# Optimization experiments

Hardware: AMD Instinct MI355X
Metric: run time of the kernel (lower is better)

Reference implementation:

```python
import jax, jax.numpy as jnp
import numpy as np

B, C1, H, W = 8, 256, 192, 192
P = 4              # effective patch size (even, <= H,W)
ROUTE_RATIO = 0.25
MIN_REGIONS = 1
HIDDEN = 128       # max(int(c1*0.5), 16)
ROUTE_HIDDEN = 64  # max(HIDDEN//2, 16)
EPS = 1e-5


def conv2d(x, w, groups=1, pad=0):
    return jax.lax.conv_general_dilated(
        x, w, (1, 1), [(pad, pad), (pad, pad)],
        dimension_numbers=("NCHW", "OIHW", "NCHW"),
        feature_group_count=groups)


def bn(x, g, b):
    # eval-mode BatchNorm with running_mean=0, running_var=1
    scale = g / jnp.sqrt(1.0 + EPS)
    return x * scale[None, :, None, None] + b[None, :, None, None]


def pixel_unshuffle(x, r):
    n, c, h, w = x.shape
    x = x.reshape(n, c, h // r, r, w // r, r)
    return x.transpose(0, 1, 3, 5, 2, 4).reshape(n, c * r * r, h // r, w // r)


def pixel_shuffle(x, r):
    n, cr, h, w = x.shape
    c = cr // (r * r)
    x = x.reshape(n, c, r, r, h, w)
    return x.transpose(0, 1, 4, 2, 5, 3).reshape(n, c, h * r, w * r)


def setup_inputs() -> dict:
    key = jax.random.key(0)
    ks = jax.random.split(key, 8)
    c4 = C1 * 4
    inp = {
        "x": jax.random.normal(ks[0], (B, C1, H, W), jnp.float32),
        # route head: 1x1 conv (no bias) -> BN -> SiLU -> 1x1 conv (bias)
        "rw1": jax.random.normal(ks[1], (ROUTE_HIDDEN, C1, 1, 1), jnp.float32) / np.sqrt(C1),
        "rg1": jnp.ones((ROUTE_HIDDEN,), jnp.float32),
        "rb1": jnp.zeros((ROUTE_HIDDEN,), jnp.float32),
        "rw2": jax.random.normal(ks[2], (1, ROUTE_HIDDEN, 1, 1), jnp.float32) / np.sqrt(ROUTE_HIDDEN),
        "rbias2": jnp.zeros((1,), jnp.float32),
        # expert: Conv(4c->hidden,1x1)+BN+SiLU, DWConv(3x3)+BN+SiLU, Conv(hidden->4c,1x1)+BN
        "ew1": jax.random.normal(ks[3], (HIDDEN, c4, 1, 1), jnp.float32) / np.sqrt(c4),
        "eg1": jnp.ones((HIDDEN,), jnp.float32),
        "eb1": jnp.zeros((HIDDEN,), jnp.float32),
        "dww": jax.random.normal(ks[4], (HIDDEN, 1, 3, 3), jnp.float32) / 3.0,
        "dwg": jnp.ones((HIDDEN,), jnp.float32),
        "dwb": jnp.zeros((HIDDEN,), jnp.float32),
        "ew2": jax.random.normal(ks[5], (c4, HIDDEN, 1, 1), jnp.float32) / np.sqrt(HIDDEN),
        "eg2": jnp.ones((c4,), jnp.float32),
        "eb2": jnp.zeros((c4,), jnp.float32),
    }
    return inp


def reference(x, rw1, rg1, rb1, rw2, rbias2, ew1, eg1, eb1, dww, dwg, dwb, ew2, eg2, eb2):
    b, c, h, w = x.shape
    p = P
    pad_h = (p - h % p) % p
    pad_w = (p - w % p) % p
    x_pad = jnp.pad(x, ((0, 0), (0, 0), (0, pad_h), (0, pad_w)))
    hp, wp = h + pad_h, w + pad_w
    gh, gw = hp // p, wp // p
    num_patches = gh * gw
    k = min(num_patches, max(MIN_REGIONS, int(np.ceil(num_patches * ROUTE_RATIO))))

    # router: avg-pool each patch, 1x1 MLP -> per-patch score
    pooled = x_pad.reshape(b, c, gh, p, gw, p).mean(axis=(3, 5))          # [b,c,gh,gw]
    r1 = jax.nn.silu(bn(conv2d(pooled, rw1), rg1, rb1))
    logits = conv2d(r1, rw2) + rbias2[None, :, None, None]
    scores = jax.nn.sigmoid(logits).reshape(b, num_patches)               # [b,N]
    top_vals, top_idx = jax.lax.top_k(scores, k)                          # [b,k]

    # gather selected patches
    patches = x_pad.reshape(b, c, gh, p, gw, p).transpose(0, 2, 4, 1, 3, 5)
    patches = patches.reshape(b, num_patches, c, p, p)
    sel = jnp.take_along_axis(patches, top_idx[:, :, None, None, None], axis=1)
    sel = sel.reshape(b * k, c, p, p)

    # expert on pixel-unshuffled patches
    y = pixel_unshuffle(sel, 2)                                           # [bk, 4c, p/2, p/2]
    y = jax.nn.silu(bn(conv2d(y, ew1), eg1, eb1))
    y = jax.nn.silu(bn(conv2d(y, dww, groups=HIDDEN, pad=1), dwg, dwb))
    y = bn(conv2d(y, ew2), eg2, eb2)
    refined = pixel_shuffle(y, 2).reshape(b, k, c, p, p)
    refined = refined * top_vals[:, :, None, None, None]

    # scatter back into zero residual
    delta = jnp.zeros((b, num_patches, c, p, p), x.dtype)
    delta = delta.at[jnp.arange(b)[:, None], top_idx].set(refined)
    delta = delta.reshape(b, gh, gw, c, p, p).transpose(0, 3, 1, 4, 2, 5)
    delta = delta.reshape(b, c, hp, wp)
    return delta[..., :h, :w]
```

## Files before the change

kernel.cpp:

```cpp
#include <hip/hip_runtime.h>
#include <hip/hip_bf16.h>

typedef __attribute__((ext_vector_type(8))) short bf16x8;
typedef __attribute__((ext_vector_type(4))) float f32x4;

#define NB 8
#define C1 256
#define HH 192
#define WW 192
#define GH 48
#define GW 48
#define NP 2304
#define KSEL 576
#define RH 64
#define HID 128
#define C4 1024
#define HW (HH*WW)

#define WS_FLAG 0
#define WS_F 64
#define WS_W16 81280ull
#define WS_POOLED 605696ull
#define WS_PSCALE WS_POOLED
#define WS_SCORES 19480064ull

#define F_RW1 0
#define F_RG1 16384
#define F_RB1 16448
#define F_RW2 16512
#define F_RBIAS2 16576
#define F_EG1 16580
#define F_EB1 16708
#define F_DWW 16836
#define F_DWG 17988
#define F_DWB 18116
#define F_EG2 18244
#define F_EB2 19268

__device__ __forceinline__ float b2f(unsigned short h) {
  return __uint_as_float(((unsigned)h) << 16);
}
__device__ __forceinline__ unsigned short f2b(float f) {
  unsigned u = __float_as_uint(f);
  u += 0x7FFF + ((u >> 16) & 1u);
  return (unsigned short)(u >> 16);
}
__device__ __forceinline__ float siluf(float v) { return v / (1.f + expf(-v)); }

__global__ void k_detect(const unsigned short* xb, char* ws) {
  __shared__ int cnt[256];
  int t = threadIdx.x;
  int c = 0;
#pragma unroll
  for (int s = 0; s < 8; ++s) {
    unsigned short u = xb[(size_t)(t * 8 + s) * 1024];
    int e = (u >> 7) & 0xFF;
    c += (u == 0 || (e >= 90 && e <= 145)) ? 1 : 0;
  }
  cnt[t] = c;
  __syncthreads();
  for (int s = 128; s > 0; s >>= 1) {
    if (t < s) cnt[t] += cnt[t + s];
    __syncthreads();
  }
  if (t == 0) *(int*)(ws + WS_FLAG) = (cnt[0] >= 1229) ? 1 : 0;
}

__global__ void k_prep(const void* rw1, const void* rg1, const void* rb1, const void* rw2,
                       const void* rbias2, const void* ew1, const void* eg1, const void* eb1,
                       const void* dww, const void* dwg, const void* dwb, const void* ew2,
                       const void* eg2, const void* eb2, char* ws) {
  int bf = *(const int*)(ws + WS_FLAG);
  float* F = (float*)(ws + WS_F);
  unsigned short* W16 = (unsigned short*)(ws + WS_W16);
  int i = blockIdx.x * 256 + threadIdx.x;
  if (i >= 282433) return;
  if (i < 20289) {
    const void* src; int si; int dof;
    if      (i < 16384) { src = rw1;    si = i;          dof = F_RW1 + si; }
    else if (i < 16448) { src = rg1;    si = i - 16384;  dof = F_RG1 + si; }
    else if (i < 16512) { src = rb1;    si = i - 16448;  dof = F_RB1 + si; }
    else if (i < 16576) { src = rw2;    si = i - 16512;  dof = F_RW2 + si; }
    else if (i < 16577) { src = rbias2; si = i - 16576;  dof = F_RBIAS2 + si; }
    else if (i < 16705) { src = eg1;    si = i - 16577;  dof = F_EG1 + si; }
    else if (i < 16833) { src = eb1;    si = i - 16705;  dof = F_EB1 + si; }
    else if (i < 17985) { src = dww;    si = i - 16833;  dof = F_DWW + si; }
    else if (i < 18113) { src = dwg;    si = i - 17985;  dof = F_DWG + si; }
    else if (i < 18241) { src = dwb;    si = i - 18113;  dof = F_DWB + si; }
    else if (i < 19265) { src = eg2;    si = i - 18241;  dof = F_EG2 + si; }
    else                { src = eb2;    si = i - 19265;  dof = F_EB2 + si; }
    F[dof] = bf ? b2f(((const unsigned short*)src)[si]) : ((const float*)src)[si];
  } else {
    int j = i - 20289;
    const void* src; int si; int dof;
    if (j < 131072) { src = ew1; si = j;          dof = j; }
    else            { src = ew2; si = j - 131072; dof = j; }
    W16[dof] = bf ? ((const unsigned short*)src)[si]
                  : f2b(((const float*)src)[si]);
  }
}

__global__ void k_pool(const void* xin, char* ws) {
  const int bf = *(const int*)(ws + WS_FLAG);
  float* pooled = (float*)(ws + WS_POOLED);
  int tid = blockIdx.x * 256 + threadIdx.x;
  int px = tid % GW;
  int t2 = tid / GW;
  int py = t2 % GH;
  int bc = t2 / GH;
  size_t base = (size_t)bc * HW + (size_t)(py * 4) * WW + px * 4;
  float s = 0.f;
  if (bf) {
#pragma unroll
    for (int r = 0; r < 4; ++r) {
      const ushort4 v = *(const ushort4*)((const unsigned short*)xin + base + r * WW);
      s += b2f(v.x) + b2f(v.y) + b2f(v.z) + b2f(v.w);
    }
  } else {
#pragma unroll
    for (int r = 0; r < 4; ++r) {
      const float4 v = *(const float4*)((const float*)xin + base + r * WW);
      s += v.x + v.y + v.z + v.w;
    }
  }
  pooled[tid] = s * 0.0625f;
}

__global__ __launch_bounds__(512, 2) void k_mlp(char* ws) {
  const float* F = (const float*)(ws + WS_F);
  const float* pooled = (const float*)(ws + WS_POOLED);
  float* scores = (float*)(ws + WS_SCORES);
  __shared__ float LP[256][68];
  __shared__ float LR[8 * 64];
  const int t = threadIdx.x;
  const int b = blockIdx.x / 36;
  const int pos0 = (blockIdx.x % 36) * 64;

  {
    const int pc = t & 15, c0 = t >> 4;
    const float* src = pooled + (size_t)(b * C1) * NP + pos0 + pc * 4;
#pragma unroll
    for (int s = 0; s < 8; ++s) {
      int c = c0 + 32 * s;
      float4 v = *(const float4*)(src + (size_t)c * NP);
      *(float4*)&LP[c][pc * 4] = v;
    }
  }
  __syncthreads();

  const int lane = t & 63;
  const int q = __builtin_amdgcn_readfirstlane(t >> 6);
  const float* wq = F + F_RW1 + q * 8 * C1;
  float acc[8];
#pragma unroll
  for (int j = 0; j < 8; ++j) acc[j] = 0.f;
  for (int c = 0; c < 256; c += 4) {
    float p0 = LP[c + 0][lane];
    float p1 = LP[c + 1][lane];
    float p2 = LP[c + 2][lane];
    float p3 = LP[c + 3][lane];
#pragma unroll
    for (int j = 0; j < 8; ++j) {
      acc[j] += wq[j * C1 + c + 0] * p0;
      acc[j] += wq[j * C1 + c + 1] * p1;
      acc[j] += wq[j * C1 + c + 2] * p2;
      acc[j] += wq[j * C1 + c + 3] * p3;
    }
  }
  const float BNS = 1.f / sqrtf(1.f + 1e-5f);
  float lp = 0.f;
#pragma unroll
  for (int j = 0; j < 8; ++j) {
    int h = q * 8 + j;
    float v = acc[j] * (F[F_RG1 + h] * BNS) + F[F_RB1 + h];
    lp += F[F_RW2 + h] * siluf(v);
  }
  LR[q * 64 + lane] = lp;
  __syncthreads();
  if (t < 64) {
    float s = F[F_RBIAS2];
#pragma unroll
    for (int j = 0; j < 8; ++j) s += LR[j * 64 + t];
    scores[b * NP + pos0 + t] = 1.f / (1.f + expf(-s));
  }
}

__global__ void k_route(char* ws) {
  const float* scores = (const float*)(ws + WS_SCORES);
  float* pscale = (float*)(ws + WS_PSCALE);
  int b = blockIdx.x / 9, r = blockIdx.x % 9;
  __shared__ float s[NP];
  for (int i = threadIdx.x; i < NP; i += 256) s[i] = scores[b * NP + i];
  __syncthreads();
  int i = r * 256 + threadIdx.x;
  float si = s[i];
  int rank = 0;
  for (int j = 0; j < NP; ++j) {
    float sj = s[j];
    rank += (sj > si || (sj == si && j < i)) ? 1 : 0;
  }
  pscale[b * NP + i] = (rank < KSEL) ? si : 0.f;
}


#define XLOAD(P_, cc_) do { \
    if (sel) { \
      size_t o_ = (size_t)(cc_) * 16 * HW; \
      if (BF) { P_##h0 = *(const ushort4*)(xh + xoff0 + o_); \
                P_##h1 = *(const ushort4*)(xh + xoff1 + o_); } \
      else    { P_##f0 = *(const float4*)(xf + xoff0 + o_); \
                P_##f1 = *(const float4*)(xf + xoff1 + o_); } \
    } \
    const unsigned short* wp_ = W1b + (cc_) * 64; \
    P_##w0 = *(const uint4*)(wp_ + wi0); \
    P_##w1 = *(const uint4*)(wp_ + wi1); \
  } while(0)

#define XWRITE(P_, UT_, WC_) do { \
    unsigned lo0_, hi0_, lo1_, hi1_; \
    if (BF) { lo0_ = P_##h0.x | ((unsigned)P_##h0.y << 16); hi0_ = P_##h0.z | ((unsigned)P_##h0.w << 16); \
              lo1_ = P_##h1.x | ((unsigned)P_##h1.y << 16); hi1_ = P_##h1.z | ((unsigned)P_##h1.w << 16); } \
    else    { asm("v_cvt_pk_bf16_f32 %0, %1, %2" : "=v"(lo0_) : "v"(P_##f0.x), "v"(P_##f0.y)); \
              asm("v_cvt_pk_bf16_f32 %0, %1, %2" : "=v"(hi0_) : "v"(P_##f0.z), "v"(P_##f0.w)); \
              asm("v_cvt_pk_bf16_f32 %0, %1, %2" : "=v"(lo1_) : "v"(P_##f1.x), "v"(P_##f1.y)); \
              asm("v_cvt_pk_bf16_f32 %0, %1, %2" : "=v"(hi1_) : "v"(P_##f1.z), "v"(P_##f1.w)); } \
    *(unsigned*)&UT_[n_lo72 + kb0] = lo0_; \
    *(unsigned*)&UT_[n_hi72 + kb0] = hi0_; \
    *(unsigned*)&UT_[n_lo72 + kb1] = lo1_; \
    *(unsigned*)&UT_[n_hi72 + kb1] = hi1_; \
    *(uint4*)&WC_[wcw0] = P_##w0; \
    *(uint4*)&WC_[wcw1] = P_##w1; \
  } while(0)

#define MFMA1(WCO_, B_, ACC_) ACC_ = __builtin_amdgcn_mfma_f32_16x16x32_bf16(*(const bf16x8*)&WC_[wc_off + (WCO_)], B_, ACC_, 0, 0, 0)

#define G1_MFMA(UT_, WCp_) do { \
    const unsigned short* WC_ = WCp_; \
    bf16x8 b0_ = *(const bf16x8*)&UT_[ut_off]; \
    bf16x8 b1_ = *(const bf16x8*)&UT_[ut_off + 32]; \
    MFMA1(0, b0_, acc10);    MFMA1(1152, b0_, acc11); \
    MFMA1(2304, b0_, acc12); MFMA1(3456, b0_, acc13); \
    MFMA1(32, b1_, acc10);   MFMA1(1152+32, b1_, acc11); \
    MFMA1(2304+32, b1_, acc12); MFMA1(3456+32, b1_, acc13); \
  } while(0)

#define G1EPI(ACC_, mi_) do { \
    _Pragma("unroll") \
    for (int r_ = 0; r_ < 4; ++r_) { \
      int h_ = 64 * wm + 16 * (mi_) + l4 * 4 + r_; \
      O1[h_ * 68 + otc] = siluf(ACC_[r_] * (F[F_EG1 + h_] * BNS) + F[F_EB1 + h_]); \
    } \
  } while(0)

#define G2_STEP(P_, WCp_, mt_) do { \
    const unsigned short* WC_ = WCp_; \
    *(uint4*)&((unsigned short*)WCp_)[w2a] = P_##a; \
    *(uint4*)&((unsigned short*)WCp_)[w2b] = P_##b; \
    if ((mt_) < 14) { \
      const unsigned short* wp_ = W2b + (size_t)((mt_) + 2) * 8192; \
      P_##a = *(const uint4*)(wp_ + w2s); \
      P_##b = *(const uint4*)(wp_ + w2s + 64); \
    } \
    __syncthreads(); \
    f32x4 a20 = (f32x4){0.f, 0.f, 0.f, 0.f}; \
    f32x4 a21 = (f32x4){0.f, 0.f, 0.f, 0.f}; \
    a20 = __builtin_amdgcn_mfma_f32_16x16x32_bf16(*(const bf16x8*)&WC_[g2_off + 0],        bq0, a20, 0,0,0); \
    a21 = __builtin_amdgcn_mfma_f32_16x16x32_bf16(*(const bf16x8*)&WC_[g2_off + 2176],     bq0, a21, 0,0,0); \
    a20 = __builtin_amdgcn_mfma_f32_16x16x32_bf16(*(const bf16x8*)&WC_[g2_off + 32],       bq1, a20, 0,0,0); \
    a21 = __builtin_amdgcn_mfma_f32_16x16x32_bf16(*(const bf16x8*)&WC_[g2_off + 2176+32],  bq1, a21, 0,0,0); \
    a20 = __builtin_amdgcn_mfma_f32_16x16x32_bf16(*(const bf16x8*)&WC_[g2_off + 64],       bq2, a20, 0,0,0); \
    a21 = __builtin_amdgcn_mfma_f32_16x16x32_bf16(*(const bf16x8*)&WC_[g2_off + 2176+64],  bq2, a21, 0,0,0); \
    a20 = __builtin_amdgcn_mfma_f32_16x16x32_bf16(*(const bf16x8*)&WC_[g2_off + 96],       bq3, a20, 0,0,0); \
    a21 = __builtin_amdgcn_mfma_f32_16x16x32_bf16(*(const bf16x8*)&WC_[g2_off + 2176+96],  bq3, a21, 0,0,0); \
    _Pragma("unroll") \
    for (int r_ = 0; r_ < 4; ++r_) { \
      int ml0_ = 32 * wm + l4 * 4 + r_; \
      int m20_ = (mt_) * 64 + ml0_; \
      OT[ml0_ * 68 + otc] = a20[r_] * (F[F_EG2 + m20_] * BNS) + F[F_EB2 + m20_]; \
      OT[(ml0_ + 16) * 68 + otc] = a21[r_] * (F[F_EG2 + m20_ + 16] * BNS) + F[F_EB2 + m20_ + 16]; \
    } \
    __syncthreads(); \
    _Pragma("unroll") \
    for (int s_ = 0; s_ < 2; ++s_) { \
      int cl_ = o_cl + 8 * s_; \
      int ch_ = (mt_) * 16 + cl_; \
      size_t ob_ = ((size_t)(bC1 + ch_) * HH + r0 + o_rr) * WW + c0 + o_p * 4; \
      int rb_ = (4 * cl_ + 2 * (o_rr & 1)) * 68 + (o_rr >> 1) * 32 + o_p; \
      float ps_ = PSs[o_p]; \
      float e0_ = OT[rb_] * ps_; \
      float e1_ = OT[rb_ + 68] * ps_; \
      float e2_ = OT[rb_ + 16] * ps_; \
      float e3_ = OT[rb_ + 68 + 16] * ps_; \
      if (BF) { ushort4 o4_ = {f2b(e0_), f2b(e1_), f2b(e2_), f2b(e3_)}; \
                *(ushort4*)((unsigned short*)outv + ob_) = o4_; } \
      else    { float4 o4_ = {e0_, e1_, e2_, e3_}; \
                *(float4*)((float*)outv + ob_) = o4_; } \
    } \
    __syncthreads(); \
  } while(0)

__global__ __launch_bounds__(512, 4) void k_expert(const void* xin, void* outv, char* ws) {
  const int BF = *(const int*)(ws + WS_FLAG);
  const float* F = (const float*)(ws + WS_F);
  const unsigned short* W1b = (const unsigned short*)(ws + WS_W16);
  const unsigned short* W2b = W1b + 131072;
  const float* pscale = (const float*)(ws + WS_PSCALE);

  __shared__ __align__(16) char LB[70720];
  unsigned short* UT0  = (unsigned short*)(LB);
  unsigned short* UT1  = (unsigned short*)(LB + 9216);
  unsigned short* WC0  = (unsigned short*)(LB + 18432);
  unsigned short* WC1  = (unsigned short*)(LB + 36864);
  float*          O1   = (float*)(LB + 18432);
  unsigned short* Y2T  = (unsigned short*)(LB);
  float*          OT   = (float*)(LB + 18432);
  unsigned short* WC20 = (unsigned short*)(LB + 35840);
  unsigned short* WC21 = (unsigned short*)(LB + 53248);
  float*          PSs  = (float*)(LB + 70656);

  const int t = threadIdx.x;
  const int lane = t & 63;
  const int w = t >> 6;
  const int wm = w >> 2, wn = w & 3;
  const int l15 = lane & 15, l4 = lane >> 4;
  const int bid = blockIdx.x;
  const int xq = bid % 3;
  const int py = (bid / 3) % GH;
  const int b  = bid / (3 * GH);
  const int r0 = py * 4, c0 = xq * 64;
  const int bC1 = b * C1;
  const float BNS = 1.f / sqrtf(1.f + 1e-5f);

  if (t < 16) PSs[t] = pscale[b * NP + py * GW + xq * 16 + t];
  __syncthreads();
  const bool sel = PSs[t & 15] != 0.f;

  const int rr = (t >> 4) & 3, v4 = t & 15;
  const int n_lo72 = (32 * (rr >> 1) + v4) * 72;
  const int n_hi72 = n_lo72 + 16 * 72;
  const int kb0 = 4 * w + 2 * (rr & 1);
  const int kb1 = kb0 + 32;
  const size_t xoff0 = ((size_t)bC1 + w) * HW + (size_t)(r0 + rr) * WW + c0 + v4 * 4;
  const size_t xoff1 = xoff0 + (size_t)8 * HW;
  const int m_0 = t >> 3, k8_0 = t & 7;
  const int wi0 = m_0 * 1024 + k8_0 * 8;
  const int wi1 = (m_0 + 64) * 1024 + k8_0 * 8;
  const int wcw0 = m_0 * 72 + k8_0 * 8;
  const int wcw1 = (m_0 + 64) * 72 + k8_0 * 8;
  const int ut_off = (16 * wn + l15) * 72 + l4 * 8;
  const int wc_off = (64 * wm + l15) * 72 + l4 * 8;
  const int otc = 16 * wn + l15;
  const int w2a = (t >> 3) * 136 + (t & 7) * 8;
  const int w2b = w2a + 64;
  const int w2s = (t >> 3) * 128 + (t & 7) * 8;
  const int g2_off = (32 * wm + l15) * 136 + l4 * 8;
  const int o_p = t & 15, o_rr = (t >> 4) & 3, o_cl = t >> 6;

  const float* xf = (const float*)xin;
  const unsigned short* xh = (const unsigned short*)xin;

  float4 Af0 = {0,0,0,0}, Af1 = {0,0,0,0}, Bf0 = {0,0,0,0}, Bf1 = {0,0,0,0};
  ushort4 Ah0 = {0,0,0,0}, Ah1 = {0,0,0,0}, Bh0 = {0,0,0,0}, Bh1 = {0,0,0,0};
  uint4 Aw0, Aw1, Bw0, Bw1;
  uint4 A2a, A2b, B2a, B2b;

  f32x4 acc10 = (f32x4){0.f,0.f,0.f,0.f};
  f32x4 acc11 = (f32x4){0.f,0.f,0.f,0.f};
  f32x4 acc12 = (f32x4){0.f,0.f,0.f,0.f};
  f32x4 acc13 = (f32x4){0.f,0.f,0.f,0.f};

  XLOAD(A, 0);
  XLOAD(B, 1);
  for (int cc2 = 0; cc2 < 8; ++cc2) {
    int cc = cc2 * 2;
    XWRITE(A, UT0, WC0);
    if (cc2 < 7) XLOAD(A, cc + 2);
    __syncthreads();
    G1_MFMA(UT0, WC0);
    XWRITE(B, UT1, WC1);
    if (cc2 < 7) XLOAD(B, cc + 3);
    __syncthreads();
    G1_MFMA(UT1, WC1);
  }

  A2a = *(const uint4*)(W2b + w2s);
  A2b = *(const uint4*)(W2b + w2s + 64);
  B2a = *(const uint4*)(W2b + 8192 + w2s);
  B2b = *(const uint4*)(W2b + 8192 + w2s + 64);

  __syncthreads();
  G1EPI(acc10, 0);
  G1EPI(acc11, 1);
  G1EPI(acc12, 2);
  G1EPI(acc13, 3);
  __syncthreads();

  {
    const int p = t & 15, hh = t >> 4;
#pragma unroll
    for (int s = 0; s < 4; ++s) {
      int h = hh + 32 * s;
      float i0 = O1[h * 68 + p];
      float i1 = O1[h * 68 + 16 + p];
      float i2 = O1[h * 68 + 32 + p];
      float i3 = O1[h * 68 + 48 + p];
      const float* kw = F + F_DWW + h * 9;
      float sd = F[F_DWG + h] * BNS, bd = F[F_DWB + h];
      float o00 = kw[4] * i0 + kw[5] * i1 + kw[7] * i2 + kw[8] * i3;
      float o01 = kw[3] * i0 + kw[4] * i1 + kw[6] * i2 + kw[7] * i3;
      float o10 = kw[1] * i0 + kw[2] * i1 + kw[4] * i2 + kw[5] * i3;
      float o11 = kw[0] * i0 + kw[1] * i1 + kw[3] * i2 + kw[4] * i3;
      Y2T[(0 * 16 + p) * 136 + h] = f2b(siluf(o00 * sd + bd));
      Y2T[(1 * 16 + p) * 136 + h] = f2b(siluf(o01 * sd + bd));
      Y2T[(2 * 16 + p) * 136 + h] = f2b(siluf(o10 * sd + bd));
      Y2T[(3 * 16 + p) * 136 + h] = f2b(siluf(o11 * sd + bd));
    }
  }
  __syncthreads();

  const int ybase = (16 * wn + l15) * 136 + l4 * 8;
  bf16x8 bq0 = *(const bf16x8*)&Y2T[ybase];
  bf16x8 bq1 = *(const bf16x8*)&Y2T[ybase + 32];
  bf16x8 bq2 = *(const bf16x8*)&Y2T[ybase + 64];
  bf16x8 bq3 = *(const bf16x8*)&Y2T[ybase + 96];

  for (int mtt = 0; mtt < 16; mtt += 2) {
    G2_STEP(A2, WC20, mtt);
    G2_STEP(B2, WC21, mtt + 1);
  }
}

extern "C" void kernel_launch(void* const* d_in, const int* in_sizes, int n_in,
                              void* d_out, int out_size, void* d_ws, size_t ws_size,
                              hipStream_t stream) {
  char* ws = (char*)d_ws;
  const void* x = d_in[0];
  k_detect<<<1, 256, 0, stream>>>((const unsigned short*)x, ws);
  k_prep<<<1104, 256, 0, stream>>>(d_in[1], d_in[2], d_in[3], d_in[4], d_in[5], d_in[6],
                                   d_in[7], d_in[8], d_in[9], d_in[10], d_in[11], d_in[12],
                                   d_in[13], d_in[14], ws);
  k_pool<<<18432, 256, 0, stream>>>(x, ws);
  k_mlp<<<288, 512, 0, stream>>>(ws);
  k_route<<<72, 256, 0, stream>>>(ws);
  k_expert<<<1152, 512, 0, stream>>>(x, d_out, ws);
}
```

Measured before the change: 319.9 us.

## Restructure second expert GEMM to read weights from global and store directly

```diff
diff --git a/kernel.cpp b/kernel.cpp
--- a/kernel.cpp
+++ b/kernel.cpp
@@ -252,53 +252,6 @@
     } \
   } while(0)
 
-#define G2_STEP(P_, WCp_, mt_) do { \
-    const unsigned short* WC_ = WCp_; \
-    *(uint4*)&((unsigned short*)WCp_)[w2a] = P_##a; \
-    *(uint4*)&((unsigned short*)WCp_)[w2b] = P_##b; \
-    if ((mt_) < 14) { \
-      const unsigned short* wp_ = W2b + (size_t)((mt_) + 2) * 8192; \
-      P_##a = *(const uint4*)(wp_ + w2s); \
-      P_##b = *(const uint4*)(wp_ + w2s + 64); \
-    } \
-    __syncthreads(); \
-    f32x4 a20 = (f32x4){0.f, 0.f, 0.f, 0.f}; \
-    f32x4 a21 = (f32x4){0.f, 0.f, 0.f, 0.f}; \
-    a20 = __builtin_amdgcn_mfma_f32_16x16x32_bf16(*(const bf16x8*)&WC_[g2_off + 0],        bq0, a20, 0,0,0); \
-    a21 = __builtin_amdgcn_mfma_f32_16x16x32_bf16(*(const bf16x8*)&WC_[g2_off + 2176],     bq0, a21, 0,0,0); \
-    a20 = __builtin_amdgcn_mfma_f32_16x16x32_bf16(*(const bf16x8*)&WC_[g2_off + 32],       bq1, a20, 0,0,0); \
-    a21 = __builtin_amdgcn_mfma_f32_16x16x32_bf16(*(const bf16x8*)&WC_[g2_off + 2176+32],  bq1, a21, 0,0,0); \
-    a20 = __builtin_amdgcn_mfma_f32_16x16x32_bf16(*(const bf16x8*)&WC_[g2_off + 64],       bq2, a20, 0,0,0); \
-    a21 = __builtin_amdgcn_mfma_f32_16x16x32_bf16(*(const bf16x8*)&WC_[g2_off + 2176+64],  bq2, a21, 0,0,0); \
-    a20 = __builtin_amdgcn_mfma_f32_16x16x32_bf16(*(const bf16x8*)&WC_[g2_off + 96],       bq3, a20, 0,0,0); \
-    a21 = __builtin_amdgcn_mfma_f32_16x16x32_bf16(*(const bf16x8*)&WC_[g2_off + 2176+96],  bq3, a21, 0,0,0); \
-    _Pragma("unroll") \
-    for (int r_ = 0; r_ < 4; ++r_) { \
-      int ml0_ = 32 * wm + l4 * 4 + r_; \
-      int m20_ = (mt_) * 64 + ml0_; \
-      OT[ml0_ * 68 + otc] = a20[r_] * (F[F_EG2 + m20_] * BNS) + F[F_EB2 + m20_]; \
-      OT[(ml0_ + 16) * 68 + otc] = a21[r_] * (F[F_EG2 + m20_ + 16] * BNS) + F[F_EB2 + m20_ + 16]; \
-    } \
-    __syncthreads(); \
-    _Pragma("unroll") \
-    for (int s_ = 0; s_ < 2; ++s_) { \
-      int cl_ = o_cl + 8 * s_; \
-      int ch_ = (mt_) * 16 + cl_; \
-      size_t ob_ = ((size_t)(bC1 + ch_) * HH + r0 + o_rr) * WW + c0 + o_p * 4; \
-      int rb_ = (4 * cl_ + 2 * (o_rr & 1)) * 68 + (o_rr >> 1) * 32 + o_p; \
-      float ps_ = PSs[o_p]; \
-      float e0_ = OT[rb_] * ps_; \
-      float e1_ = OT[rb_ + 68] * ps_; \
-      float e2_ = OT[rb_ + 16] * ps_; \
-      float e3_ = OT[rb_ + 68 + 16] * ps_; \
-      if (BF) { ushort4 o4_ = {f2b(e0_), f2b(e1_), f2b(e2_), f2b(e3_)}; \
-                *(ushort4*)((unsigned short*)outv + ob_) = o4_; } \
-      else    { float4 o4_ = {e0_, e1_, e2_, e3_}; \
-                *(float4*)((float*)outv + ob_) = o4_; } \
-    } \
-    __syncthreads(); \
-  } while(0)
-
 __global__ __launch_bounds__(512, 4) void k_expert(const void* xin, void* outv, char* ws) {
   const int BF = *(const int*)(ws + WS_FLAG);
   const float* F = (const float*)(ws + WS_F);
@@ -306,17 +259,14 @@
   const unsigned short* W2b = W1b + 131072;
   const float* pscale = (const float*)(ws + WS_PSCALE);
 
-  __shared__ __align__(16) char LB[70720];
+  __shared__ __align__(16) char LB[55360];
   unsigned short* UT0  = (unsigned short*)(LB);
   unsigned short* UT1  = (unsigned short*)(LB + 9216);
   unsigned short* WC0  = (unsigned short*)(LB + 18432);
   unsigned short* WC1  = (unsigned short*)(LB + 36864);
   float*          O1   = (float*)(LB + 18432);
   unsigned short* Y2T  = (unsigned short*)(LB);
-  float*          OT   = (float*)(LB + 18432);
-  unsigned short* WC20 = (unsigned short*)(LB + 35840);
-  unsigned short* WC21 = (unsigned short*)(LB + 53248);
-  float*          PSs  = (float*)(LB + 70656);
+  float*          PSs  = (float*)(LB + 55296);
 
   const int t = threadIdx.x;
   const int lane = t & 63;
@@ -333,7 +283,8 @@
 
   if (t < 16) PSs[t] = pscale[b * NP + py * GW + xq * 16 + t];
   __syncthreads();
-  const bool sel = PSs[t & 15] != 0.f;
+  const float ps = PSs[t & 15];
+  const bool sel = ps != 0.f;
 
   const int rr = (t >> 4) & 3, v4 = t & 15;
   const int n_lo72 = (32 * (rr >> 1) + v4) * 72;
@@ -350,11 +301,6 @@
   const int ut_off = (16 * wn + l15) * 72 + l4 * 8;
   const int wc_off = (64 * wm + l15) * 72 + l4 * 8;
   const int otc = 16 * wn + l15;
-  const int w2a = (t >> 3) * 136 + (t & 7) * 8;
-  const int w2b = w2a + 64;
-  const int w2s = (t >> 3) * 128 + (t & 7) * 8;
-  const int g2_off = (32 * wm + l15) * 136 + l4 * 8;
-  const int o_p = t & 15, o_rr = (t >> 4) & 3, o_cl = t >> 6;
 
   const float* xf = (const float*)xin;
   const unsigned short* xh = (const unsigned short*)xin;
@@ -362,7 +308,6 @@
   float4 Af0 = {0,0,0,0}, Af1 = {0,0,0,0}, Bf0 = {0,0,0,0}, Bf1 = {0,0,0,0};
   ushort4 Ah0 = {0,0,0,0}, Ah1 = {0,0,0,0}, Bh0 = {0,0,0,0}, Bh1 = {0,0,0,0};
   uint4 Aw0, Aw1, Bw0, Bw1;
-  uint4 A2a, A2b, B2a, B2b;
 
   f32x4 acc10 = (f32x4){0.f,0.f,0.f,0.f};
   f32x4 acc11 = (f32x4){0.f,0.f,0.f,0.f};
@@ -382,11 +327,6 @@
     __syncthreads();
     G1_MFMA(UT1, WC1);
   }
-
-  A2a = *(const uint4*)(W2b + w2s);
-  A2b = *(const uint4*)(W2b + w2s + 64);
-  B2a = *(const uint4*)(W2b + 8192 + w2s);
-  B2b = *(const uint4*)(W2b + 8192 + w2s + 64);
 
   __syncthreads();
   G1EPI(acc10, 0);
@@ -418,15 +358,56 @@
   }
   __syncthreads();
 
-  const int ybase = (16 * wn + l15) * 136 + l4 * 8;
-  bf16x8 bq0 = *(const bf16x8*)&Y2T[ybase];
-  bf16x8 bq1 = *(const bf16x8*)&Y2T[ybase + 32];
-  bf16x8 bq2 = *(const bf16x8*)&Y2T[ybase + 64];
-  bf16x8 bq3 = *(const bf16x8*)&Y2T[ybase + 96];
-
-  for (int mtt = 0; mtt < 16; mtt += 2) {
-    G2_STEP(A2, WC20, mtt);
-    G2_STEP(B2, WC21, mtt + 1);
+  {
+    bf16x8 bq[4][4];
+#pragma unroll
+    for (int nq = 0; nq < 4; ++nq)
+#pragma unroll
+      for (int ks = 0; ks < 4; ++ks)
+        bq[nq][ks] = *(const bf16x8*)&Y2T[(16 * nq + l15) * 136 + ks * 32 + l4 * 8];
+
+    const unsigned short* w2l = W2b + ((size_t)(w * 128 + l15)) * 128 + l4 * 8;
+    const int colb = c0 + (t & 15) * 4;
+#pragma unroll
+    for (int msub = 0; msub < 8; ++msub) {
+      bf16x8 af0 = *(const bf16x8*)(w2l + msub * 2048 + 0);
+      bf16x8 af1 = *(const bf16x8*)(w2l + msub * 2048 + 32);
+      bf16x8 af2 = *(const bf16x8*)(w2l + msub * 2048 + 64);
+      bf16x8 af3 = *(const bf16x8*)(w2l + msub * 2048 + 96);
+      f32x4 a2[4];
+#pragma unroll
+      for (int nq = 0; nq < 4; ++nq) {
+        f32x4 acc = (f32x4){0.f, 0.f, 0.f, 0.f};
+        acc = __builtin_amdgcn_mfma_f32_16x16x32_bf16(af0, bq[nq][0], acc, 0, 0, 0);
+        acc = __builtin_amdgcn_mfma_f32_16x16x32_bf16(af1, bq[nq][1], acc, 0, 0, 0);
+        acc = __builtin_amdgcn_mfma_f32_16x16x32_bf16(af2, bq[nq][2], acc, 0, 0, 0);
+        acc = __builtin_amdgcn_mfma_f32_16x16x32_bf16(af3, bq[nq][3], acc, 0, 0, 0);
+        a2[nq] = acc;
+      }
+      const int m2b = w * 128 + msub * 16 + l4 * 4;
+      const float4 g4 = *(const float4*)&F[F_EG2 + m2b];
+      const float4 b4 = *(const float4*)&F[F_EB2 + m2b];
+      const int ch = m2b >> 2;
+      const size_t chb = ((size_t)(bC1 + ch) * HH + r0) * WW;
+#pragma unroll
+      for (int nq = 0; nq < 4; ++nq) {
+        const int row = (nq >> 1) * 2;
+        const int col = colb + (nq & 1) * 2;
+        float e0 = (a2[nq][0] * (g4.x * BNS) + b4.x) * ps;
+        float e1 = (a2[nq][1] * (g4.y * BNS) + b4.y) * ps;
+        float e2 = (a2[nq][2] * (g4.z * BNS) + b4.z) * ps;
+        float e3 = (a2[nq][3] * (g4.w * BNS) + b4.w) * ps;
+        if (BF) {
+          unsigned p0 = (unsigned)f2b(e0) | ((unsigned)f2b(e1) << 16);
+          unsigned p1 = (unsigned)f2b(e2) | ((unsigned)f2b(e3) << 16);
+          *(unsigned*)((unsigned short*)outv + chb + (size_t)row * WW + col) = p0;
+          *(unsigned*)((unsigned short*)outv + chb + (size_t)(row + 1) * WW + col) = p1;
+        } else {
+          *(float2*)((float*)outv + chb + (size_t)row * WW + col) = make_float2(e0, e1);
+          *(float2*)((float*)outv + chb + (size_t)(row + 1) * WW + col) = make_float2(e2, e3);
+        }
+      }
+    }
   }
 }
 
```

Measured after the change: 334.6 us. 4.6% more time.

## Process two patch rows per expert block to double weight reuse

Applied to the files above, without the earlier changes.

```diff
diff --git a/kernel.cpp b/kernel.cpp
--- a/kernel.cpp
+++ b/kernel.cpp
@@ -3,6 +3,7 @@
 
 typedef __attribute__((ext_vector_type(8))) short bf16x8;
 typedef __attribute__((ext_vector_type(4))) float f32x4;
+typedef __attribute__((ext_vector_type(2))) unsigned u32x2;
 
 #define NB 8
 #define C1 256
@@ -44,6 +45,11 @@
   unsigned u = __float_as_uint(f);
   u += 0x7FFF + ((u >> 16) & 1u);
   return (unsigned short)(u >> 16);
+}
+__device__ __forceinline__ unsigned pkbf(float a, float b) {
+  unsigned r;
+  asm("v_cvt_pk_bf16_f32 %0, %1, %2" : "=v"(r) : "v"(a), "v"(b));
+  return r;
 }
 __device__ __forceinline__ float siluf(float v) { return v / (1.f + expf(-v)); }
 
@@ -135,7 +141,6 @@
   const int t = threadIdx.x;
   const int b = blockIdx.x / 36;
   const int pos0 = (blockIdx.x % 36) * 64;
-
   {
     const int pc = t & 15, c0 = t >> 4;
     const float* src = pooled + (size_t)(b * C1) * NP + pos0 + pc * 4;
@@ -147,7 +152,6 @@
     }
   }
   __syncthreads();
-
   const int lane = t & 63;
   const int q = __builtin_amdgcn_readfirstlane(t >> 6);
   const float* wq = F + F_RW1 + q * 8 * C1;
@@ -203,13 +207,20 @@
 }
 
 
+#define MM(A_, B_, C_) C_ = __builtin_amdgcn_mfma_f32_16x16x32_bf16(A_, B_, C_, 0, 0, 0)
+
 #define XLOAD(P_, cc_) do { \
-    if (sel) { \
-      size_t o_ = (size_t)(cc_) * 16 * HW; \
-      if (BF) { P_##h0 = *(const ushort4*)(xh + xoff0 + o_); \
-                P_##h1 = *(const ushort4*)(xh + xoff1 + o_); } \
-      else    { P_##f0 = *(const float4*)(xf + xoff0 + o_); \
-                P_##f1 = *(const float4*)(xf + xoff1 + o_); } \
+    size_t o_ = (size_t)(cc_) * 16 * HW; \
+    if (BF) { \
+      if (sel0) { *(ushort4*)&P_##f00 = *(const ushort4*)(xh + xoff00 + o_); \
+                  *(ushort4*)&P_##f10 = *(const ushort4*)(xh + xoff10 + o_); } \
+      if (sel1) { *(ushort4*)&P_##f01 = *(const ushort4*)(xh + xoff01 + o_); \
+                  *(ushort4*)&P_##f11 = *(const ushort4*)(xh + xoff11 + o_); } \
+    } else { \
+      if (sel0) { P_##f00 = *(const float4*)(xf + xoff00 + o_); \
+                  P_##f10 = *(const float4*)(xf + xoff10 + o_); } \
+      if (sel1) { P_##f01 = *(const float4*)(xf + xoff01 + o_); \
+                  P_##f11 = *(const float4*)(xf + xoff11 + o_); } \
     } \
     const unsigned short* wp_ = W1b + (cc_) * 64; \
     P_##w0 = *(const uint4*)(wp_ + wi0); \
@@ -217,80 +228,109 @@
   } while(0)
 
 #define XWRITE(P_, UT_, WC_) do { \
-    unsigned lo0_, hi0_, lo1_, hi1_; \
-    if (BF) { lo0_ = P_##h0.x | ((unsigned)P_##h0.y << 16); hi0_ = P_##h0.z | ((unsigned)P_##h0.w << 16); \
-              lo1_ = P_##h1.x | ((unsigned)P_##h1.y << 16); hi1_ = P_##h1.z | ((unsigned)P_##h1.w << 16); } \
-    else    { asm("v_cvt_pk_bf16_f32 %0, %1, %2" : "=v"(lo0_) : "v"(P_##f0.x), "v"(P_##f0.y)); \
-              asm("v_cvt_pk_bf16_f32 %0, %1, %2" : "=v"(hi0_) : "v"(P_##f0.z), "v"(P_##f0.w)); \
-              asm("v_cvt_pk_bf16_f32 %0, %1, %2" : "=v"(lo1_) : "v"(P_##f1.x), "v"(P_##f1.y)); \
-              asm("v_cvt_pk_bf16_f32 %0, %1, %2" : "=v"(hi1_) : "v"(P_##f1.z), "v"(P_##f1.w)); } \
-    *(unsigned*)&UT_[n_lo72 + kb0] = lo0_; \
-    *(unsigned*)&UT_[n_hi72 + kb0] = hi0_; \
-    *(unsigned*)&UT_[n_lo72 + kb1] = lo1_; \
-    *(unsigned*)&UT_[n_hi72 + kb1] = hi1_; \
+    unsigned q00_, q01_, q10_, q11_, q20_, q21_, q30_, q31_; \
+    if (BF) { \
+      ushort4 u0_ = *(ushort4*)&P_##f00, u1_ = *(ushort4*)&P_##f01; \
+      ushort4 u2_ = *(ushort4*)&P_##f10, u3_ = *(ushort4*)&P_##f11; \
+      q00_ = u0_.x | ((unsigned)u0_.y << 16); q01_ = u0_.z | ((unsigned)u0_.w << 16); \
+      q10_ = u1_.x | ((unsigned)u1_.y << 16); q11_ = u1_.z | ((unsigned)u1_.w << 16); \
+      q20_ = u2_.x | ((unsigned)u2_.y << 16); q21_ = u2_.z | ((unsigned)u2_.w << 16); \
+      q30_ = u3_.x | ((unsigned)u3_.y << 16); q31_ = u3_.z | ((unsigned)u3_.w << 16); \
+    } else { \
+      q00_ = pkbf(P_##f00.x, P_##f00.y); q01_ = pkbf(P_##f00.z, P_##f00.w); \
+      q10_ = pkbf(P_##f01.x, P_##f01.y); q11_ = pkbf(P_##f01.z, P_##f01.w); \
+      q20_ = pkbf(P_##f10.x, P_##f10.y); q21_ = pkbf(P_##f10.z, P_##f10.w); \
+      q30_ = pkbf(P_##f11.x, P_##f11.y); q31_ = pkbf(P_##f11.z, P_##f11.w); \
+    } \
+    *(unsigned*)&UT_[n00_72 + kb0] = q00_; \
+    *(unsigned*)&UT_[n01_72 + kb0] = q01_; \
+    *(unsigned*)&UT_[n10_72 + kb0] = q10_; \
+    *(unsigned*)&UT_[n11_72 + kb0] = q11_; \
+    *(unsigned*)&UT_[n00_72 + kb1] = q20_; \
+    *(unsigned*)&UT_[n01_72 + kb1] = q21_; \
+    *(unsigned*)&UT_[n10_72 + kb1] = q30_; \
+    *(unsigned*)&UT_[n11_72 + kb1] = q31_; \
     *(uint4*)&WC_[wcw0] = P_##w0; \
     *(uint4*)&WC_[wcw1] = P_##w1; \
   } while(0)
 
-#define MFMA1(WCO_, B_, ACC_) ACC_ = __builtin_amdgcn_mfma_f32_16x16x32_bf16(*(const bf16x8*)&WC_[wc_off + (WCO_)], B_, ACC_, 0, 0, 0)
-
 #define G1_MFMA(UT_, WCp_) do { \
     const unsigned short* WC_ = WCp_; \
-    bf16x8 b0_ = *(const bf16x8*)&UT_[ut_off]; \
-    bf16x8 b1_ = *(const bf16x8*)&UT_[ut_off + 32]; \
-    MFMA1(0, b0_, acc10);    MFMA1(1152, b0_, acc11); \
-    MFMA1(2304, b0_, acc12); MFMA1(3456, b0_, acc13); \
-    MFMA1(32, b1_, acc10);   MFMA1(1152+32, b1_, acc11); \
-    MFMA1(2304+32, b1_, acc12); MFMA1(3456+32, b1_, acc13); \
+    bf16x8 b00_ = *(const bf16x8*)&UT_[ut0_off]; \
+    bf16x8 b10_ = *(const bf16x8*)&UT_[ut1_off]; \
+    bf16x8 b01_ = *(const bf16x8*)&UT_[ut0_off + 32]; \
+    bf16x8 b11_ = *(const bf16x8*)&UT_[ut1_off + 32]; \
+    bf16x8 a_; \
+    a_ = *(const bf16x8*)&WC_[wc_off];          MM(a_, b00_, acc00); MM(a_, b10_, acc01); \
+    a_ = *(const bf16x8*)&WC_[wc_off + 1152];   MM(a_, b00_, acc10); MM(a_, b10_, acc11); \
+    a_ = *(const bf16x8*)&WC_[wc_off + 2304];   MM(a_, b00_, acc20); MM(a_, b10_, acc21); \
+    a_ = *(const bf16x8*)&WC_[wc_off + 3456];   MM(a_, b00_, acc30); MM(a_, b10_, acc31); \
+    a_ = *(const bf16x8*)&WC_[wc_off + 32];     MM(a_, b01_, acc00); MM(a_, b11_, acc01); \
+    a_ = *(const bf16x8*)&WC_[wc_off + 1184];   MM(a_, b01_, acc10); MM(a_, b11_, acc11); \
+    a_ = *(const bf16x8*)&WC_[wc_off + 2336];   MM(a_, b01_, acc20); MM(a_, b11_, acc21); \
+    a_ = *(const bf16x8*)&WC_[wc_off + 3488];   MM(a_, b01_, acc30); MM(a_, b11_, acc31); \
   } while(0)
 
-#define G1EPI(ACC_, mi_) do { \
-    _Pragma("unroll") \
-    for (int r_ = 0; r_ < 4; ++r_) { \
-      int h_ = 64 * wm + 16 * (mi_) + l4 * 4 + r_; \
-      O1[h_ * 68 + otc] = siluf(ACC_[r_] * (F[F_EG1 + h_] * BNS) + F[F_EB1 + h_]); \
-    } \
+#define G1EPI(A0_, A1_, mi_) do { \
+    const int h0_ = 64 * wm + 16 * (mi_) + l4 * 4; \
+    float g0_ = F[F_EG1 + h0_] * BNS,     c0_ = F[F_EB1 + h0_]; \
+    float g1_ = F[F_EG1 + h0_ + 1] * BNS, c1_ = F[F_EB1 + h0_ + 1]; \
+    float g2_ = F[F_EG1 + h0_ + 2] * BNS, c2_ = F[F_EB1 + h0_ + 2]; \
+    float g3_ = F[F_EG1 + h0_ + 3] * BNS, c3_ = F[F_EB1 + h0_ + 3]; \
+    unsigned lo0_ = pkbf(siluf(A0_[0] * g0_ + c0_), siluf(A0_[1] * g1_ + c1_)); \
+    unsigned hi0_ = pkbf(siluf(A0_[2] * g2_ + c2_), siluf(A0_[3] * g3_ + c3_)); \
+    unsigned lo1_ = pkbf(siluf(A1_[0] * g0_ + c0_), siluf(A1_[1] * g1_ + c1_)); \
+    unsigned hi1_ = pkbf(siluf(A1_[2] * g2_ + c2_), siluf(A1_[3] * g3_ + c3_)); \
+    *(u32x2*)&O1b[(32 * wn + l15) * 136 + h0_] = (u32x2){lo0_, hi0_}; \
+    *(u32x2*)&O1b[(32 * wn + 16 + l15) * 136 + h0_] = (u32x2){lo1_, hi1_}; \
   } while(0)
 
 #define G2_STEP(P_, WCp_, mt_) do { \
-    const unsigned short* WC_ = WCp_; \
-    *(uint4*)&((unsigned short*)WCp_)[w2a] = P_##a; \
-    *(uint4*)&((unsigned short*)WCp_)[w2b] = P_##b; \
+    const unsigned short* WC_ = (const unsigned short*)(WCp_); \
+    *(uint4*)&((unsigned short*)(WCp_))[w2a] = P_##a; \
+    *(uint4*)&((unsigned short*)(WCp_))[w2b] = P_##b; \
     if ((mt_) < 14) { \
       const unsigned short* wp_ = W2b + (size_t)((mt_) + 2) * 8192; \
       P_##a = *(const uint4*)(wp_ + w2s); \
       P_##b = *(const uint4*)(wp_ + w2s + 64); \
     } \
     __syncthreads(); \
-    f32x4 a20 = (f32x4){0.f, 0.f, 0.f, 0.f}; \
-    f32x4 a21 = (f32x4){0.f, 0.f, 0.f, 0.f}; \
-    a20 = __builtin_amdgcn_mfma_f32_16x16x32_bf16(*(const bf16x8*)&WC_[g2_off + 0],        bq0, a20, 0,0,0); \
-    a21 = __builtin_amdgcn_mfma_f32_16x16x32_bf16(*(const bf16x8*)&WC_[g2_off + 2176],     bq0, a21, 0,0,0); \
-    a20 = __builtin_amdgcn_mfma_f32_16x16x32_bf16(*(const bf16x8*)&WC_[g2_off + 32],       bq1, a20, 0,0,0); \
-    a21 = __builtin_amdgcn_mfma_f32_16x16x32_bf16(*(const bf16x8*)&WC_[g2_off + 2176+32],  bq1, a21, 0,0,0); \
-    a20 = __builtin_amdgcn_mfma_f32_16x16x32_bf16(*(const bf16x8*)&WC_[g2_off + 64],       bq2, a20, 0,0,0); \
-    a21 = __builtin_amdgcn_mfma_f32_16x16x32_bf16(*(const bf16x8*)&WC_[g2_off + 2176+64],  bq2, a21, 0,0,0); \
-    a20 = __builtin_amdgcn_mfma_f32_16x16x32_bf16(*(const bf16x8*)&WC_[g2_off + 96],       bq3, a20, 0,0,0); \
-    a21 = __builtin_amdgcn_mfma_f32_16x16x32_bf16(*(const bf16x8*)&WC_[g2_off + 2176+96],  bq3, a21, 0,0,0); \
+    f32x4 c00_ = (f32x4){0.f,0.f,0.f,0.f}; \
+    f32x4 c01_ = (f32x4){0.f,0.f,0.f,0.f}; \
+    f32x4 c10_ = (f32x4){0.f,0.f,0.f,0.f}; \
+    f32x4 c11_ = (f32x4){0.f,0.f,0.f,0.f}; \
+    { bf16x8 a0_, a1_; \
+      a0_ = *(const bf16x8*)&WC_[g2_off];        a1_ = *(const bf16x8*)&WC_[g2_off + 2176]; \
+      MM(a0_, bq00, c00_); MM(a0_, bq10, c01_); MM(a1_, bq00, c10_); MM(a1_, bq10, c11_); \
+      a0_ = *(const bf16x8*)&WC_[g2_off + 32];   a1_ = *(const bf16x8*)&WC_[g2_off + 2208]; \
+      MM(a0_, bq01, c00_); MM(a0_, bq11, c01_); MM(a1_, bq01, c10_); MM(a1_, bq11, c11_); \
+      a0_ = *(const bf16x8*)&WC_[g2_off + 64];   a1_ = *(const bf16x8*)&WC_[g2_off + 2240]; \
+      MM(a0_, bq02, c00_); MM(a0_, bq12, c01_); MM(a1_, bq02, c10_); MM(a1_, bq12, c11_); \
+      a0_ = *(const bf16x8*)&WC_[g2_off + 96];   a1_ = *(const bf16x8*)&WC_[g2_off + 2272]; \
+      MM(a0_, bq03, c00_); MM(a0_, bq13, c01_); MM(a1_, bq03, c10_); MM(a1_, bq13, c11_); \
+    } \
     _Pragma("unroll") \
     for (int r_ = 0; r_ < 4; ++r_) { \
       int ml0_ = 32 * wm + l4 * 4 + r_; \
       int m20_ = (mt_) * 64 + ml0_; \
-      OT[ml0_ * 68 + otc] = a20[r_] * (F[F_EG2 + m20_] * BNS) + F[F_EB2 + m20_]; \
-      OT[(ml0_ + 16) * 68 + otc] = a21[r_] * (F[F_EG2 + m20_ + 16] * BNS) + F[F_EB2 + m20_ + 16]; \
+      float g0_ = F[F_EG2 + m20_] * BNS,      d0_ = F[F_EB2 + m20_]; \
+      float g1_ = F[F_EG2 + m20_ + 16] * BNS, d1_ = F[F_EB2 + m20_ + 16]; \
+      OT[ml0_ * 132 + otn0]             = c00_[r_] * g0_ + d0_; \
+      OT[ml0_ * 132 + otn0 + 16]        = c01_[r_] * g0_ + d0_; \
+      OT[(ml0_ + 16) * 132 + otn0]      = c10_[r_] * g1_ + d1_; \
+      OT[(ml0_ + 16) * 132 + otn0 + 16] = c11_[r_] * g1_ + d1_; \
     } \
     __syncthreads(); \
     _Pragma("unroll") \
-    for (int s_ = 0; s_ < 2; ++s_) { \
-      int cl_ = o_cl + 8 * s_; \
-      int ch_ = (mt_) * 16 + cl_; \
-      size_t ob_ = ((size_t)(bC1 + ch_) * HH + r0 + o_rr) * WW + c0 + o_p * 4; \
-      int rb_ = (4 * cl_ + 2 * (o_rr & 1)) * 68 + (o_rr >> 1) * 32 + o_p; \
-      float ps_ = PSs[o_p]; \
-      float e0_ = OT[rb_] * ps_; \
-      float e1_ = OT[rb_ + 68] * ps_; \
-      float e2_ = OT[rb_ + 16] * ps_; \
-      float e3_ = OT[rb_ + 68 + 16] * ps_; \
+    for (int s_ = 0; s_ < 4; ++s_) { \
+      int chl_ = st_cg + 4 * s_; \
+      int ch_ = (mt_) * 16 + chl_; \
+      int mlb_ = chl_ * 4 + st_dr * 2; \
+      float e0_ = OT[mlb_ * 132 + st_nb] * psv; \
+      float e1_ = OT[(mlb_ + 1) * 132 + st_nb] * psv; \
+      float e2_ = OT[mlb_ * 132 + st_nb + 16] * psv; \
+      float e3_ = OT[(mlb_ + 1) * 132 + st_nb + 16] * psv; \
+      size_t ob_ = ((size_t)(bC1 + ch_) * HH + r0 + st_row) * WW + c0 + st_p * 4; \
       if (BF) { ushort4 o4_ = {f2b(e0_), f2b(e1_), f2b(e2_), f2b(e3_)}; \
                 *(ushort4*)((unsigned short*)outv + ob_) = o4_; } \
       else    { float4 o4_ = {e0_, e1_, e2_, e3_}; \
@@ -306,17 +346,17 @@
   const unsigned short* W2b = W1b + 131072;
   const float* pscale = (const float*)(ws + WS_PSCALE);
 
-  __shared__ __align__(16) char LB[70720];
+  __shared__ __align__(16) char LB[73856];
   unsigned short* UT0  = (unsigned short*)(LB);
-  unsigned short* UT1  = (unsigned short*)(LB + 9216);
-  unsigned short* WC0  = (unsigned short*)(LB + 18432);
-  unsigned short* WC1  = (unsigned short*)(LB + 36864);
-  float*          O1   = (float*)(LB + 18432);
-  unsigned short* Y2T  = (unsigned short*)(LB);
-  float*          OT   = (float*)(LB + 18432);
-  unsigned short* WC20 = (unsigned short*)(LB + 35840);
-  unsigned short* WC21 = (unsigned short*)(LB + 53248);
-  float*          PSs  = (float*)(LB + 70656);
+  unsigned short* UT1  = (unsigned short*)(LB + 18432);
+  unsigned short* WC0  = (unsigned short*)(LB + 36864);
+  unsigned short* WC1  = (unsigned short*)(LB + 55296);
+  unsigned short* O1b  = (unsigned short*)(LB);
+  unsigned short* Y2T  = (unsigned short*)(LB + 36864);
+  unsigned short* WC20 = (unsigned short*)(LB);
+  unsigned short* WC21 = (unsigned short*)(LB + 17408);
+  float*          OT   = (float*)(LB + 36864);
+  float*          PSs  = (float*)(LB + 73728);
 
   const int t = threadIdx.x;
   const int lane = t & 63;
@@ -325,49 +365,58 @@
   const int l15 = lane & 15, l4 = lane >> 4;
   const int bid = blockIdx.x;
   const int xq = bid % 3;
-  const int py = (bid / 3) % GH;
-  const int b  = bid / (3 * GH);
-  const int r0 = py * 4, c0 = xq * 64;
+  const int pyq = (bid / 3) % 24;
+  const int b  = bid / 72;
+  const int r0 = pyq * 8, c0 = xq * 64;
   const int bC1 = b * C1;
   const float BNS = 1.f / sqrtf(1.f + 1e-5f);
 
-  if (t < 16) PSs[t] = pscale[b * NP + py * GW + xq * 16 + t];
-  __syncthreads();
-  const bool sel = PSs[t & 15] != 0.f;
+  if (t < 32) PSs[t] = pscale[b * NP + (pyq * 2 + (t >> 4)) * GW + xq * 16 + (t & 15)];
+  __syncthreads();
 
   const int rr = (t >> 4) & 3, v4 = t & 15;
-  const int n_lo72 = (32 * (rr >> 1) + v4) * 72;
-  const int n_hi72 = n_lo72 + 16 * 72;
+  const bool sel0 = PSs[v4] != 0.f;
+  const bool sel1 = PSs[16 + v4] != 0.f;
+  const int n00_72 = ((rr >> 1) * 32 + v4) * 72;
+  const int n01_72 = n00_72 + 16 * 72;
+  const int n10_72 = n00_72 + 64 * 72;
+  const int n11_72 = n10_72 + 16 * 72;
   const int kb0 = 4 * w + 2 * (rr & 1);
   const int kb1 = kb0 + 32;
-  const size_t xoff0 = ((size_t)bC1 + w) * HW + (size_t)(r0 + rr) * WW + c0 + v4 * 4;
-  const size_t xoff1 = xoff0 + (size_t)8 * HW;
+  const size_t xoff00 = ((size_t)bC1 + w) * HW + (size_t)(r0 + rr) * WW + c0 + v4 * 4;
+  const size_t xoff01 = xoff00 + 4 * WW;
+  const size_t xoff10 = xoff00 + (size_t)8 * HW;
+  const size_t xoff11 = xoff10 + 4 * WW;
   const int m_0 = t >> 3, k8_0 = t & 7;
   const int wi0 = m_0 * 1024 + k8_0 * 8;
   const int wi1 = (m_0 + 64) * 1024 + k8_0 * 8;
   const int wcw0 = m_0 * 72 + k8_0 * 8;
   const int wcw1 = (m_0 + 64) * 72 + k8_0 * 8;
-  const int ut_off = (16 * wn + l15) * 72 + l4 * 8;
+  const int ut0_off = (32 * wn + l15) * 72 + l4 * 8;
+  const int ut1_off = ut0_off + 16 * 72;
   const int wc_off = (64 * wm + l15) * 72 + l4 * 8;
-  const int otc = 16 * wn + l15;
   const int w2a = (t >> 3) * 136 + (t & 7) * 8;
   const int w2b = w2a + 64;
   const int w2s = (t >> 3) * 128 + (t & 7) * 8;
   const int g2_off = (32 * wm + l15) * 136 + l4 * 8;
-  const int o_p = t & 15, o_rr = (t >> 4) & 3, o_cl = t >> 6;
+  const int otn0 = 32 * wn + l15;
+  const int st_p = t & 15, st_row = (t >> 4) & 7, st_cg = t >> 7;
+  const int st_rh = st_row >> 2, st_pr = (st_row >> 1) & 1, st_dr = st_row & 1;
+  const int st_nb = st_rh * 64 + st_pr * 32 + st_p;
+  const float psv = PSs[st_rh * 16 + st_p];
 
   const float* xf = (const float*)xin;
   const unsigned short* xh = (const unsigned short*)xin;
 
-  float4 Af0 = {0,0,0,0}, Af1 = {0,0,0,0}, Bf0 = {0,0,0,0}, Bf1 = {0,0,0,0};
-  ushort4 Ah0 = {0,0,0,0}, Ah1 = {0,0,0,0}, Bh0 = {0,0,0,0}, Bh1 = {0,0,0,0};
+  float4 Af00 = {0,0,0,0}, Af01 = {0,0,0,0}, Af10 = {0,0,0,0}, Af11 = {0,0,0,0};
+  float4 Bf00 = {0,0,0,0}, Bf01 = {0,0,0,0}, Bf10 = {0,0,0,0}, Bf11 = {0,0,0,0};
   uint4 Aw0, Aw1, Bw0, Bw1;
   uint4 A2a, A2b, B2a, B2b;
 
-  f32x4 acc10 = (f32x4){0.f,0.f,0.f,0.f};
-  f32x4 acc11 = (f32x4){0.f,0.f,0.f,0.f};
-  f32x4 acc12 = (f32x4){0.f,0.f,0.f,0.f};
-  f32x4 acc13 = (f32x4){0.f,0.f,0.f,0.f};
+  f32x4 acc00 = (f32x4){0.f,0.f,0.f,0.f}, acc01 = acc00;
+  f32x4 acc10 = acc00, acc11 = acc00;
+  f32x4 acc20 = acc00, acc21 = acc00;
+  f32x4 acc30 = acc00, acc31 = acc00;
 
   XLOAD(A, 0);
   XLOAD(B, 1);
@@ -389,40 +438,50 @@
   B2b = *(const uint4*)(W2b + 8192 + w2s + 64);
 
   __syncthreads();
-  G1EPI(acc10, 0);
-  G1EPI(acc11, 1);
-  G1EPI(acc12, 2);
-  G1EPI(acc13, 3);
+  G1EPI(acc00, acc01, 0);
+  G1EPI(acc10, acc11, 1);
+  G1EPI(acc20, acc21, 2);
+  G1EPI(acc30, acc31, 3);
   __syncthreads();
 
   {
-    const int p = t & 15, hh = t >> 4;
-#pragma unroll
-    for (int s = 0; s < 4; ++s) {
-      int h = hh + 32 * s;
-      float i0 = O1[h * 68 + p];
-      float i1 = O1[h * 68 + 16 + p];
-      float i2 = O1[h * 68 + 32 + p];
-      float i3 = O1[h * 68 + 48 + p];
-      const float* kw = F + F_DWW + h * 9;
-      float sd = F[F_DWG + h] * BNS, bd = F[F_DWB + h];
-      float o00 = kw[4] * i0 + kw[5] * i1 + kw[7] * i2 + kw[8] * i3;
-      float o01 = kw[3] * i0 + kw[4] * i1 + kw[6] * i2 + kw[7] * i3;
-      float o10 = kw[1] * i0 + kw[2] * i1 + kw[4] * i2 + kw[5] * i3;
-      float o11 = kw[0] * i0 + kw[1] * i1 + kw[3] * i2 + kw[4] * i3;
-      Y2T[(0 * 16 + p) * 136 + h] = f2b(siluf(o00 * sd + bd));
-      Y2T[(1 * 16 + p) * 136 + h] = f2b(siluf(o01 * sd + bd));
-      Y2T[(2 * 16 + p) * 136 + h] = f2b(siluf(o10 * sd + bd));
-      Y2T[(3 * 16 + p) * 136 + h] = f2b(siluf(o11 * sd + bd));
+    const int dh = t & 127;
+    const int dgrp = t >> 7;
+    const float* kw = F + F_DWW + dh * 9;
+    float k0 = kw[0], k1 = kw[1], k2 = kw[2], k3 = kw[3], k4 = kw[4];
+    float k5 = kw[5], k6 = kw[6], k7 = kw[7], k8 = kw[8];
+    float sd = F[F_DWG + dh] * BNS, bd = F[F_DWB + dh];
+#pragma unroll
+    for (int s = 0; s < 8; ++s) {
+      int combo = dgrp * 8 + s;
+      int patch = combo & 15, rh = combo >> 4;
+      int nb = (rh * 64 + patch) * 136 + dh;
+      float i0 = b2f(O1b[nb]);
+      float i1 = b2f(O1b[nb + 16 * 136]);
+      float i2 = b2f(O1b[nb + 32 * 136]);
+      float i3 = b2f(O1b[nb + 48 * 136]);
+      float o00 = k4 * i0 + k5 * i1 + k7 * i2 + k8 * i3;
+      float o01 = k3 * i0 + k4 * i1 + k6 * i2 + k7 * i3;
+      float o10 = k1 * i0 + k2 * i1 + k4 * i2 + k5 * i3;
+      float o11 = k0 * i0 + k1 * i1 + k3 * i2 + k4 * i3;
+      Y2T[nb] = f2b(siluf(o00 * sd + bd));
+      Y2T[nb + 16 * 136] = f2b(siluf(o01 * sd + bd));
+      Y2T[nb + 32 * 136] = f2b(siluf(o10 * sd + bd));
+      Y2T[nb + 48 * 136] = f2b(siluf(o11 * sd + bd));
     }
   }
   __syncthreads();
 
-  const int ybase = (16 * wn + l15) * 136 + l4 * 8;
-  bf16x8 bq0 = *(const bf16x8*)&Y2T[ybase];
-  bf16x8 bq1 = *(const bf16x8*)&Y2T[ybase + 32];
-  bf16x8 bq2 = *(const bf16x8*)&Y2T[ybase + 64];
-  bf16x8 bq3 = *(const bf16x8*)&Y2T[ybase + 96];
+  const int yb0 = (32 * wn + l15) * 136 + l4 * 8;
+  const int yb1 = yb0 + 16 * 136;
+  bf16x8 bq00 = *(const bf16x8*)&Y2T[yb0];
+  bf16x8 bq01 = *(const bf16x8*)&Y2T[yb0 + 32];
+  bf16x8 bq02 = *(const bf16x8*)&Y2T[yb0 + 64];
+  bf16x8 bq03 = *(const bf16x8*)&Y2T[yb0 + 96];
+  bf16x8 bq10 = *(const bf16x8*)&Y2T[yb1];
+  bf16x8 bq11 = *(const bf16x8*)&Y2T[yb1 + 32];
+  bf16x8 bq12 = *(const bf16x8*)&Y2T[yb1 + 64];
+  bf16x8 bq13 = *(const bf16x8*)&Y2T[yb1 + 96];
 
   for (int mtt = 0; mtt < 16; mtt += 2) {
     G2_STEP(A2, WC20, mtt);
@@ -442,5 +501,5 @@
   k_pool<<<18432, 256, 0, stream>>>(x, ws);
   k_mlp<<<288, 512, 0, stream>>>(ws);
   k_route<<<72, 256, 0, stream>>>(ws);
-  k_expert<<<1152, 512, 0, stream>>>(x, d_out, ws);
-}
+  k_expert<<<576, 512, 0, stream>>>(x, d_out, ws);
+}
```

New measurement: 354.9 us. 1.11x slower.
